# Kernel tuning notes

Hardware: AMD Instinct MI355X
Metric: run time of the kernel (lower is better)

## Reference

```python
import jax, jax.numpy as jnp
import numpy as np

EPS = 1e-8


def setup_inputs() -> dict:
    key = jax.random.key(0)
    ks = jax.random.split(key, 7)
    B, H, S, D = 4, 16, 4096, 64
    query = jax.random.normal(ks[0], (B, H, S, D), dtype=jnp.float32)
    k_in = jax.random.normal(ks[1], (B, H, S, D), dtype=jnp.float32)
    value = jax.random.normal(ks[2], (B, H, S, D), dtype=jnp.float32)
    output = jax.random.normal(ks[3], (B, H, S, D), dtype=jnp.float32)
    betas = jax.random.normal(ks[4], (H, 1, D), dtype=jnp.float32)
    init_states = jax.random.normal(ks[5], (H, D, D), dtype=jnp.float32)
    init_z = jax.random.uniform(ks[6], (H, D), dtype=jnp.float32)
    return {"query": query, "key": k_in, "value": value, "output": output,
            "betas": betas, "init_states": init_states, "init_z": init_z}


def reference(query, key, value, output, betas, init_states, init_z):
    # ---- compute updates (delta rule) ----
    sigma_k = jax.nn.elu(key) + 1.0                       # [B,H,S,D]
    # retrieved_value = (sigma_k @ states) / (sigma_k @ z + eps)
    num = jnp.einsum('bhsd,hde->bhse', sigma_k, init_states)   # [B,H,S,D]
    den = jnp.einsum('bhsd,hd->bhs', sigma_k, init_z)[..., None] + EPS
    value_update = value - num / den                      # delta rule
    # memory_states = init_states + sigma_k^T @ value_update -> [B,H,D,D]
    memory_states = init_states[None] + jnp.einsum('bhsd,bhse->bhde', sigma_k, value_update)
    memory_z = init_z[None] + sigma_k.sum(axis=-2)        # [B,H,D]
    # ---- retrieve memory ----
    sigma_q = jax.nn.elu(query) + 1.0                     # [B,H,S,D]
    retrieved = jnp.einsum('bhsd,bhde->bhse', sigma_q, memory_states)
    norm = jnp.einsum('bhsd,bhd->bhs', sigma_q, memory_z)[..., None] + EPS
    memory_output = retrieved / norm                      # [B,H,S,D]
    # ---- sigmoid-gated blend ----
    gate = jax.nn.sigmoid(betas)                          # [H,1,D] broadcasts over B,S
    return gate * memory_output + (1.0 - gate) * output
```

## Files before the change

kernel.cpp:

```cpp
#include <hip/hip_runtime.h>
#include <hip/hip_bf16.h>


#define B_  4
#define H_  16
#define S_  4096
#define D_  64
#define BH_ 64
#define EPS_ 1e-8f

typedef __attribute__((ext_vector_type(8))) short bf16x8;
typedef __attribute__((ext_vector_type(4))) float f32x4;
typedef __attribute__((ext_vector_type(4))) unsigned short u16x4;

__device__ __forceinline__ unsigned short f2bf(float x) {
    union { float f; unsigned u; } v; v.f = x;
    return (unsigned short)((v.u + 0x7FFFu + ((v.u >> 16) & 1u)) >> 16);
}
__device__ __forceinline__ float elup1(float x) {
    return x > 0.0f ? x + 1.0f : __expf(x);
}
__device__ __forceinline__ f32x4 fzero() { f32x4 z = {0.f, 0.f, 0.f, 0.f}; return z; }

__global__ __launch_bounds__(256, 4) void k1_states(
    const float* __restrict__ Kp, const float* __restrict__ Vp,
    const float* __restrict__ W0, const float* __restrict__ Z0,
    float* __restrict__ Mpart, float* __restrict__ Zpart, int NS)
{
    const int bh = blockIdx.x / NS;
    const int p  = blockIdx.x % NS;
    const int h  = bh & (H_ - 1);
    const int tid  = threadIdx.x;
    const int lane = tid & 63;
    const int wave = tid >> 6;
    const int c16  = lane & 15;
    const int g4   = lane >> 4;

    __shared__ float Glds[4][16][68];

    int   col[4];
    float z0l[4];
    #pragma unroll
    for (int q = 0; q < 4; ++q) {
        col[q] = (((wave + q) & 3) << 4) + c16;
        z0l[q] = Z0[h * 64 + col[q]];
    }

    bf16x8 ones;
    #pragma unroll
    for (int j = 0; j < 8; ++j) ones[j] = (short)0x3F80;

    const size_t base   = (size_t)bh * S_ * D_;
    const int    schunk = S_ / NS;
    const int    nch    = schunk >> 5;

    f32x4 mp1[4], gac[4], zac = fzero();
    #pragma unroll
    for (int i = 0; i < 4; ++i) { mp1[i] = fzero(); gac[i] = fzero(); }

    #pragma unroll 1
    for (int c = wave; c < nch; c += 4) {
        const float* kr = Kp + base + (size_t)(p * schunk + c * 32) * D_;
        const float* vr = Vp + base + (size_t)(p * schunk + c * 32) * D_;

        float kf[4][8];
        #pragma unroll
        for (int q = 0; q < 4; ++q)
        #pragma unroll
        for (int j = 0; j < 8; ++j)
            kf[q][j] = kr[(g4 * 8 + j) * 64 + col[q]];

        float den[8];
        #pragma unroll
        for (int j = 0; j < 8; ++j) den[j] = 0.f;
        #pragma unroll
        for (int q = 0; q < 4; ++q)
        #pragma unroll
        for (int j = 0; j < 8; ++j) {
            float s = elup1(kf[q][j]);
            kf[q][j] = s;
            den[j] += s * z0l[q];
        }
        #pragma unroll
        for (int j = 0; j < 8; ++j) {
            float d = den[j];
            d += __shfl_xor(d, 1); d += __shfl_xor(d, 2);
            d += __shfl_xor(d, 4); d += __shfl_xor(d, 8);
            den[j] = __builtin_amdgcn_rcpf(d + EPS_);
        }

        bf16x8 aown, skbS[4];
        #pragma unroll
        for (int j = 0; j < 8; ++j) aown[j] = (short)f2bf(kf[0][j]);
        #pragma unroll
        for (int q = 0; q < 4; ++q)
        #pragma unroll
        for (int j = 0; j < 8; ++j)
            skbS[q][j] = (short)f2bf(kf[q][j] * den[j]);

        float vf[4][8];
        #pragma unroll
        for (int nt = 0; nt < 4; ++nt)
        #pragma unroll
        for (int j = 0; j < 8; ++j)
            vf[nt][j] = vr[(g4 * 8 + j) * 64 + nt * 16 + c16];
        bf16x8 vbf[4];
        #pragma unroll
        for (int nt = 0; nt < 4; ++nt)
        #pragma unroll
        for (int j = 0; j < 8; ++j) vbf[nt][j] = (short)f2bf(vf[nt][j]);

        zac = __builtin_amdgcn_mfma_f32_16x16x32_bf16(aown, ones, zac, 0, 0, 0);
        #pragma unroll
        for (int nt = 0; nt < 4; ++nt)
            mp1[nt] = __builtin_amdgcn_mfma_f32_16x16x32_bf16(aown, vbf[nt], mp1[nt], 0, 0, 0);
        #pragma unroll
        for (int q = 0; q < 4; ++q)
            gac[q] = __builtin_amdgcn_mfma_f32_16x16x32_bf16(aown, skbS[q], gac[q], 0, 0, 0);
    }

    #pragma unroll
    for (int q = 0; q < 4; ++q)
    #pragma unroll
    for (int r = 0; r < 4; ++r)
        Glds[wave][g4 * 4 + r][(((wave + q) & 3) << 4) + c16] = gac[q][r];

    bf16x8 ag[2];
    #pragma unroll
    for (int kk = 0; kk < 2; ++kk)
    #pragma unroll
    for (int j = 0; j < 8; ++j)
        ag[kk][j] = (short)f2bf(Glds[wave][c16][kk * 32 + g4 * 8 + j]);

    f32x4 gw[4];
    #pragma unroll
    for (int nt = 0; nt < 4; ++nt) {
        f32x4 t = fzero();
        #pragma unroll
        for (int kk = 0; kk < 2; ++kk) {
            bf16x8 wb;
            #pragma unroll
            for (int j = 0; j < 8; ++j)
                wb[j] = (short)f2bf(W0[(size_t)h * 4096 + (kk * 32 + g4 * 8 + j) * 64 + nt * 16 + c16]);
            t = __builtin_amdgcn_mfma_f32_16x16x32_bf16(ag[kk], wb, t, 0, 0, 0);
        }
        gw[nt] = t;
    }

    #pragma unroll
    for (int nt = 0; nt < 4; ++nt)
    #pragma unroll
    for (int r = 0; r < 4; ++r)
        Glds[wave][g4 * 4 + r][nt * 16 + c16] = mp1[nt][r] - gw[nt][r];

    float* mout = Mpart + ((size_t)p * BH_ + bh) * 4096 + wave * 1024;
    #pragma unroll
    for (int q2 = 0; q2 < 4; ++q2) {
        f32x4 v = *(const f32x4*)&Glds[wave][q2 * 4 + g4][c16 * 4];
        *(f32x4*)(mout + q2 * 256 + lane * 4) = v;
    }

    if (c16 == 0) {
        #pragma unroll
        for (int r = 0; r < 4; ++r)
            Zpart[((size_t)p * BH_ + bh) * 64 + wave * 16 + g4 * 4 + r] = zac[r];
    }
}

__global__ void k_reduce(const float* __restrict__ Mpart, const float* __restrict__ Zpart,
                         const float* __restrict__ W0, const float* __restrict__ Z0,
                         unsigned short* __restrict__ MfinT, float* __restrict__ Zfin, int NS)
{
    const int bh = blockIdx.x >> 2, q = blockIdx.x & 3;
    const int h = bh & (H_ - 1), t = threadIdx.x;
    __shared__ float Ml[16][65];

    const int o = q * 1024 + t * 4;
    f32x4 s = *(const f32x4*)(W0 + (size_t)h * 4096 + o);
    for (int p = 0; p < NS; ++p)
        s = s + *(const f32x4*)(Mpart + ((size_t)p * BH_ + bh) * 4096 + o);
    const int dl = t >> 4, e0 = (t & 15) * 4;
    #pragma unroll
    for (int j = 0; j < 4; ++j) Ml[dl][e0 + j] = s[j];
    __syncthreads();

    const int e = t >> 2, dd0 = (t & 3) * 4;
    u16x4 w;
    #pragma unroll
    for (int j = 0; j < 4; ++j) w[j] = f2bf(Ml[dd0 + j][e]);
    *(u16x4*)(MfinT + (size_t)bh * 4096 + e * 64 + q * 16 + dd0) = w;

    if (q == 0 && t < 64) {
        float zs = Z0[h * 64 + t];
        for (int p = 0; p < NS; ++p) zs += Zpart[((size_t)p * BH_ + bh) * 64 + t];
        Zfin[bh * 64 + t] = zs;
    }
}

__global__ __launch_bounds__(256, 4) void k2_out(
    const float* __restrict__ Qp, const float* __restrict__ Op,
    const float* __restrict__ Bp, const unsigned short* __restrict__ MfinT,
    const float* __restrict__ Zfin, float* __restrict__ Out, int NS2)
{
    const int bh = blockIdx.x / NS2;
    const int p  = blockIdx.x % NS2;
    const int h  = bh & (H_ - 1);
    const int tid = threadIdx.x, lane = tid & 63, wave = tid >> 6;
    const int c16 = lane & 15, g4 = lane >> 4;

    float mzv[2][8];
    #pragma unroll
    for (int kk = 0; kk < 2; ++kk) {
        f32x4 a = *(const f32x4*)(Zfin + bh * 64 + kk * 32 + g4 * 8);
        f32x4 b = *(const f32x4*)(Zfin + bh * 64 + kk * 32 + g4 * 8 + 4);
        #pragma unroll
        for (int j = 0; j < 4; ++j) { mzv[kk][j] = a[j]; mzv[kk][4 + j] = b[j]; }
    }

    bf16x8 mf[4][2];
    #pragma unroll
    for (int et = 0; et < 4; ++et)
    #pragma unroll
    for (int kk = 0; kk < 2; ++kk)
        mf[et][kk] = *(const bf16x8*)(MfinT + (size_t)bh * 4096 + (et * 16 + c16) * 64 + kk * 32 + g4 * 8);

    float gate[4][4];
    #pragma unroll
    for (int et = 0; et < 4; ++et)
    #pragma unroll
    for (int r = 0; r < 4; ++r) {
        float b = Bp[h * 64 + et * 16 + g4 * 4 + r];
        gate[et][r] = 1.0f / (1.0f + __expf(-b));
    }

    const size_t base = (size_t)bh * S_ * D_;
    const int schunk = S_ / NS2, ngroups = schunk / 32;

    for (int g = wave; g < ngroups; g += 4) {
        const int row0 = p * schunk + g * 32;

        float sq[2][2][8];
        #pragma unroll
        for (int st = 0; st < 2; ++st) {
            const float* qr = Qp + base + (size_t)(row0 + st * 16 + c16) * D_;
            #pragma unroll
            for (int kk = 0; kk < 2; ++kk) {
                f32x4 a = *(const f32x4*)(qr + kk * 32 + g4 * 8);
                f32x4 b = *(const f32x4*)(qr + kk * 32 + g4 * 8 + 4);
                #pragma unroll
                for (int j = 0; j < 4; ++j) {
                    sq[st][kk][j]     = elup1(a[j]);
                    sq[st][kk][4 + j] = elup1(b[j]);
                }
            }
        }

        float n0 = 0.f, n1 = 0.f;
        #pragma unroll
        for (int kk = 0; kk < 2; ++kk)
        #pragma unroll
        for (int j = 0; j < 8; ++j) {
            n0 += sq[0][kk][j] * mzv[kk][j];
            n1 += sq[1][kk][j] * mzv[kk][j];
        }
        n0 += __shfl_xor(n0, 16); n0 += __shfl_xor(n0, 32);
        n1 += __shfl_xor(n1, 16); n1 += __shfl_xor(n1, 32);
        const float rn0 = __builtin_amdgcn_rcpf(n0 + EPS_);
        const float rn1 = __builtin_amdgcn_rcpf(n1 + EPS_);

        bf16x8 sqf[2][2];
        #pragma unroll
        for (int st = 0; st < 2; ++st)
        #pragma unroll
        for (int kk = 0; kk < 2; ++kk) {
            bf16x8 f;
            #pragma unroll
            for (int j = 0; j < 8; ++j) f[j] = (short)f2bf(sq[st][kk][j]);
            sqf[st][kk] = f;
        }

        f32x4 acc[2][4];
        #pragma unroll
        for (int st = 0; st < 2; ++st)
        #pragma unroll
        for (int et = 0; et < 4; ++et) {
            f32x4 t = __builtin_amdgcn_mfma_f32_16x16x32_bf16(mf[et][0], sqf[st][0], fzero(), 0, 0, 0);
            acc[st][et] = __builtin_amdgcn_mfma_f32_16x16x32_bf16(mf[et][1], sqf[st][1], t, 0, 0, 0);
        }

        #pragma unroll
        for (int st = 0; st < 2; ++st) {
            const float rn = st ? rn1 : rn0;
            const size_t roff = base + (size_t)(row0 + st * 16 + c16) * D_;
            #pragma unroll
            for (int et = 0; et < 4; ++et) {
                f32x4 o4 = *(const f32x4*)(Op + roff + et * 16 + g4 * 4);
                f32x4 w;
                #pragma unroll
                for (int r = 0; r < 4; ++r) {
                    float t = acc[st][et][r] * rn;
                    w[r] = o4[r] + gate[et][r] * (t - o4[r]);
                }
                *(f32x4*)(Out + roff + et * 16 + g4 * 4) = w;
            }
        }
    }
}

extern "C" void kernel_launch(void* const* d_in, const int* in_sizes, int n_in,
                              void* d_out, int out_size, void* d_ws, size_t ws_size,
                              hipStream_t stream)
{
    const float* Q  = (const float*)d_in[0];
    const float* K  = (const float*)d_in[1];
    const float* V  = (const float*)d_in[2];
    const float* O  = (const float*)d_in[3];
    const float* Bt = (const float*)d_in[4];
    const float* W0 = (const float*)d_in[5];
    const float* Z0 = (const float*)d_in[6];
    float* Out = (float*)d_out;

    int NS = 16;
    auto need = [](int ns) -> size_t {
        return sizeof(float) * ((size_t)ns * BH_ * 4096 + (size_t)ns * BH_ * 64 + BH_ * 64) +
               sizeof(unsigned short) * (size_t)BH_ * 4096;
    };
    while (NS > 1 && need(NS) > ws_size) NS >>= 1;

    float* Mpart = (float*)d_ws;
    float* Zpart = Mpart + (size_t)NS * BH_ * 4096;
    float* Zfin  = Zpart + (size_t)NS * BH_ * 64;
    unsigned short* MfinT = (unsigned short*)(Zfin + (size_t)BH_ * 64);

    hipLaunchKernelGGL(k1_states, dim3(BH_ * NS), dim3(256), 0, stream,
                       K, V, W0, Z0, Mpart, Zpart, NS);
    hipLaunchKernelGGL(k_reduce, dim3(BH_ * 4), dim3(256), 0, stream,
                       Mpart, Zpart, W0, Z0, MfinT, Zfin, NS);
    hipLaunchKernelGGL(k2_out, dim3(BH_ * 32), dim3(256), 0, stream,
                       Q, O, Bt, MfinT, Zfin, Out, 32);
}
```

Baseline: 89.18 us.

## Split kernels into single-wave blocks and hoist loads for memory-level parallelism

Both the state-accumulation kernel and the output kernel now launch 64-thread single-wave blocks, with four times as many blocks, instead of 256-thread blocks. The state kernel hoists the value loads ahead of the elu/denominator math and processes two chunks per loop iteration. The output kernel gives each wave one 32-row group and issues all query and output loads up front. The aim is more independent blocks and more loads in flight to hide memory latency, at the cost of more block-scheduling overhead and higher register pressure.

```diff
diff --git a/kernel.cpp b/kernel.cpp
--- a/kernel.cpp
+++ b/kernel.cpp
@@ -22,27 +22,28 @@
 }
 __device__ __forceinline__ f32x4 fzero() { f32x4 z = {0.f, 0.f, 0.f, 0.f}; return z; }
 
-__global__ __launch_bounds__(256, 4) void k1_states(
+__global__ __launch_bounds__(64, 4) void k1_states(
     const float* __restrict__ Kp, const float* __restrict__ Vp,
     const float* __restrict__ W0, const float* __restrict__ Z0,
     float* __restrict__ Mpart, float* __restrict__ Zpart, int NS)
 {
-    const int bh = blockIdx.x / NS;
-    const int p  = blockIdx.x % NS;
-    const int h  = bh & (H_ - 1);
-    const int tid  = threadIdx.x;
-    const int lane = tid & 63;
-    const int wave = tid >> 6;
+    const int bid = blockIdx.x;
+    const int w   = bid & 3;
+    const int t2  = bid >> 2;
+    const int bh  = t2 / NS;
+    const int p   = t2 % NS;
+    const int h   = bh & (H_ - 1);
+    const int lane = threadIdx.x;
     const int c16  = lane & 15;
     const int g4   = lane >> 4;
 
-    __shared__ float Glds[4][16][68];
+    __shared__ float Glds[16][68];
 
     int   col[4];
     float z0l[4];
     #pragma unroll
     for (int q = 0; q < 4; ++q) {
-        col[q] = (((wave + q) & 3) << 4) + c16;
+        col[q] = (((w + q) & 3) << 4) + c16;
         z0l[q] = Z0[h * 64 + col[q]];
     }
 
@@ -58,8 +59,7 @@
     #pragma unroll
     for (int i = 0; i < 4; ++i) { mp1[i] = fzero(); gac[i] = fzero(); }
 
-    #pragma unroll 1
-    for (int c = wave; c < nch; c += 4) {
+    auto do_chunk = [&](int c) {
         const float* kr = Kp + base + (size_t)(p * schunk + c * 32) * D_;
         const float* vr = Vp + base + (size_t)(p * schunk + c * 32) * D_;
 
@@ -69,6 +69,13 @@
         #pragma unroll
         for (int j = 0; j < 8; ++j)
             kf[q][j] = kr[(g4 * 8 + j) * 64 + col[q]];
+
+        float vf[4][8];
+        #pragma unroll
+        for (int nt = 0; nt < 4; ++nt)
+        #pragma unroll
+        for (int j = 0; j < 8; ++j)
+            vf[nt][j] = vr[(g4 * 8 + j) * 64 + nt * 16 + c16];
 
         float den[8];
         #pragma unroll
@@ -98,12 +105,6 @@
         for (int j = 0; j < 8; ++j)
             skbS[q][j] = (short)f2bf(kf[q][j] * den[j]);
 
-        float vf[4][8];
-        #pragma unroll
-        for (int nt = 0; nt < 4; ++nt)
-        #pragma unroll
-        for (int j = 0; j < 8; ++j)
-            vf[nt][j] = vr[(g4 * 8 + j) * 64 + nt * 16 + c16];
         bf16x8 vbf[4];
         #pragma unroll
         for (int nt = 0; nt < 4; ++nt)
@@ -117,20 +118,26 @@
         #pragma unroll
         for (int q = 0; q < 4; ++q)
             gac[q] = __builtin_amdgcn_mfma_f32_16x16x32_bf16(aown, skbS[q], gac[q], 0, 0, 0);
+    };
+
+    #pragma unroll 1
+    for (int c = w; c < nch; c += 8) {
+        do_chunk(c);
+        if (c + 4 < nch) do_chunk(c + 4);
     }
 
     #pragma unroll
     for (int q = 0; q < 4; ++q)
     #pragma unroll
     for (int r = 0; r < 4; ++r)
-        Glds[wave][g4 * 4 + r][(((wave + q) & 3) << 4) + c16] = gac[q][r];
+        Glds[g4 * 4 + r][(((w + q) & 3) << 4) + c16] = gac[q][r];
 
     bf16x8 ag[2];
     #pragma unroll
     for (int kk = 0; kk < 2; ++kk)
     #pragma unroll
     for (int j = 0; j < 8; ++j)
-        ag[kk][j] = (short)f2bf(Glds[wave][c16][kk * 32 + g4 * 8 + j]);
+        ag[kk][j] = (short)f2bf(Glds[c16][kk * 32 + g4 * 8 + j]);
 
     f32x4 gw[4];
     #pragma unroll
@@ -151,19 +158,19 @@
     for (int nt = 0; nt < 4; ++nt)
     #pragma unroll
     for (int r = 0; r < 4; ++r)
-        Glds[wave][g4 * 4 + r][nt * 16 + c16] = mp1[nt][r] - gw[nt][r];
-
-    float* mout = Mpart + ((size_t)p * BH_ + bh) * 4096 + wave * 1024;
+        Glds[g4 * 4 + r][nt * 16 + c16] = mp1[nt][r] - gw[nt][r];
+
+    float* mout = Mpart + ((size_t)p * BH_ + bh) * 4096 + w * 1024;
     #pragma unroll
     for (int q2 = 0; q2 < 4; ++q2) {
-        f32x4 v = *(const f32x4*)&Glds[wave][q2 * 4 + g4][c16 * 4];
+        f32x4 v = *(const f32x4*)&Glds[q2 * 4 + g4][c16 * 4];
         *(f32x4*)(mout + q2 * 256 + lane * 4) = v;
     }
 
     if (c16 == 0) {
         #pragma unroll
         for (int r = 0; r < 4; ++r)
-            Zpart[((size_t)p * BH_ + bh) * 64 + wave * 16 + g4 * 4 + r] = zac[r];
+            Zpart[((size_t)p * BH_ + bh) * 64 + w * 16 + g4 * 4 + r] = zac[r];
     }
 }
 
@@ -197,16 +204,44 @@
     }
 }
 
-__global__ __launch_bounds__(256, 4) void k2_out(
+__global__ __launch_bounds__(64, 4) void k2_out(
     const float* __restrict__ Qp, const float* __restrict__ Op,
     const float* __restrict__ Bp, const unsigned short* __restrict__ MfinT,
-    const float* __restrict__ Zfin, float* __restrict__ Out, int NS2)
+    const float* __restrict__ Zfin, float* __restrict__ Out)
 {
-    const int bh = blockIdx.x / NS2;
-    const int p  = blockIdx.x % NS2;
-    const int h  = bh & (H_ - 1);
-    const int tid = threadIdx.x, lane = tid & 63, wave = tid >> 6;
+    const int bid = blockIdx.x;
+    const int bh  = bid >> 7;
+    const int g   = bid & 127;
+    const int h   = bh & (H_ - 1);
+    const int lane = threadIdx.x;
     const int c16 = lane & 15, g4 = lane >> 4;
+    const int row0 = g * 32;
+    const size_t base = (size_t)bh * S_ * D_;
+
+    float sq[2][2][8];
+    #pragma unroll
+    for (int st = 0; st < 2; ++st) {
+        const float* qr = Qp + base + (size_t)(row0 + st * 16 + c16) * D_;
+        #pragma unroll
+        for (int kk = 0; kk < 2; ++kk) {
+            f32x4 a = *(const f32x4*)(qr + kk * 32 + g4 * 8);
+            f32x4 b = *(const f32x4*)(qr + kk * 32 + g4 * 8 + 4);
+            #pragma unroll
+            for (int j = 0; j < 4; ++j) {
+                sq[st][kk][j]     = a[j];
+                sq[st][kk][4 + j] = b[j];
+            }
+        }
+    }
+
+    f32x4 o4[2][4];
+    #pragma unroll
+    for (int st = 0; st < 2; ++st) {
+        const float* orow = Op + base + (size_t)(row0 + st * 16 + c16) * D_;
+        #pragma unroll
+        for (int et = 0; et < 4; ++et)
+            o4[st][et] = *(const f32x4*)(orow + et * 16 + g4 * 4);
+    }
 
     float mzv[2][8];
     #pragma unroll
@@ -216,14 +251,12 @@
         #pragma unroll
         for (int j = 0; j < 4; ++j) { mzv[kk][j] = a[j]; mzv[kk][4 + j] = b[j]; }
     }
-
     bf16x8 mf[4][2];
     #pragma unroll
     for (int et = 0; et < 4; ++et)
     #pragma unroll
     for (int kk = 0; kk < 2; ++kk)
         mf[et][kk] = *(const bf16x8*)(MfinT + (size_t)bh * 4096 + (et * 16 + c16) * 64 + kk * 32 + g4 * 8);
-
     float gate[4][4];
     #pragma unroll
     for (int et = 0; et < 4; ++et)
@@ -233,76 +266,55 @@
         gate[et][r] = 1.0f / (1.0f + __expf(-b));
     }
 
-    const size_t base = (size_t)bh * S_ * D_;
-    const int schunk = S_ / NS2, ngroups = schunk / 32;
-
-    for (int g = wave; g < ngroups; g += 4) {
-        const int row0 = p * schunk + g * 32;
-
-        float sq[2][2][8];
-        #pragma unroll
-        for (int st = 0; st < 2; ++st) {
-            const float* qr = Qp + base + (size_t)(row0 + st * 16 + c16) * D_;
+    float n0 = 0.f, n1 = 0.f;
+    #pragma unroll
+    for (int st = 0; st < 2; ++st)
+    #pragma unroll
+    for (int kk = 0; kk < 2; ++kk)
+    #pragma unroll
+    for (int j = 0; j < 8; ++j) {
+        float s = elup1(sq[st][kk][j]);
+        sq[st][kk][j] = s;
+        if (st == 0) n0 += s * mzv[kk][j]; else n1 += s * mzv[kk][j];
+    }
+    n0 += __shfl_xor(n0, 16); n0 += __shfl_xor(n0, 32);
+    n1 += __shfl_xor(n1, 16); n1 += __shfl_xor(n1, 32);
+    const float rn0 = __builtin_amdgcn_rcpf(n0 + EPS_);
+    const float rn1 = __builtin_amdgcn_rcpf(n1 + EPS_);
+
+    bf16x8 sqf[2][2];
+    #pragma unroll
+    for (int st = 0; st < 2; ++st)
+    #pragma unroll
+    for (int kk = 0; kk < 2; ++kk) {
+        bf16x8 f;
+        #pragma unroll
+        for (int j = 0; j < 8; ++j) f[j] = (short)f2bf(sq[st][kk][j]);
+        sqf[st][kk] = f;
+    }
+
+    f32x4 acc[2][4];
+    #pragma unroll
+    for (int st = 0; st < 2; ++st)
+    #pragma unroll
+    for (int et = 0; et < 4; ++et) {
+        f32x4 t = __builtin_amdgcn_mfma_f32_16x16x32_bf16(mf[et][0], sqf[st][0], fzero(), 0, 0, 0);
+        acc[st][et] = __builtin_amdgcn_mfma_f32_16x16x32_bf16(mf[et][1], sqf[st][1], t, 0, 0, 0);
+    }
+
+    #pragma unroll
+    for (int st = 0; st < 2; ++st) {
+        const float rn = st ? rn1 : rn0;
+        const size_t roff = base + (size_t)(row0 + st * 16 + c16) * D_;
+        #pragma unroll
+        for (int et = 0; et < 4; ++et) {
+            f32x4 wv;
             #pragma unroll
-            for (int kk = 0; kk < 2; ++kk) {
-                f32x4 a = *(const f32x4*)(qr + kk * 32 + g4 * 8);
-                f32x4 b = *(const f32x4*)(qr + kk * 32 + g4 * 8 + 4);
-                #pragma unroll
-                for (int j = 0; j < 4; ++j) {
-                    sq[st][kk][j]     = elup1(a[j]);
-                    sq[st][kk][4 + j] = elup1(b[j]);
-                }
+            for (int r = 0; r < 4; ++r) {
+                float t = acc[st][et][r] * rn;
+                wv[r] = o4[st][et][r] + gate[et][r] * (t - o4[st][et][r]);
             }
-        }
-
-        float n0 = 0.f, n1 = 0.f;
-        #pragma unroll
-        for (int kk = 0; kk < 2; ++kk)
-        #pragma unroll
-        for (int j = 0; j < 8; ++j) {
-            n0 += sq[0][kk][j] * mzv[kk][j];
-            n1 += sq[1][kk][j] * mzv[kk][j];
-        }
-        n0 += __shfl_xor(n0, 16); n0 += __shfl_xor(n0, 32);
-        n1 += __shfl_xor(n1, 16); n1 += __shfl_xor(n1, 32);
-        const float rn0 = __builtin_amdgcn_rcpf(n0 + EPS_);
-        const float rn1 = __builtin_amdgcn_rcpf(n1 + EPS_);
-
-        bf16x8 sqf[2][2];
-        #pragma unroll
-        for (int st = 0; st < 2; ++st)
-        #pragma unroll
-        for (int kk = 0; kk < 2; ++kk) {
-            bf16x8 f;
-            #pragma unroll
-            for (int j = 0; j < 8; ++j) f[j] = (short)f2bf(sq[st][kk][j]);
-            sqf[st][kk] = f;
-        }
-
-        f32x4 acc[2][4];
-        #pragma unroll
-        for (int st = 0; st < 2; ++st)
-        #pragma unroll
-        for (int et = 0; et < 4; ++et) {
-            f32x4 t = __builtin_amdgcn_mfma_f32_16x16x32_bf16(mf[et][0], sqf[st][0], fzero(), 0, 0, 0);
-            acc[st][et] = __builtin_amdgcn_mfma_f32_16x16x32_bf16(mf[et][1], sqf[st][1], t, 0, 0, 0);
-        }
-
-        #pragma unroll
-        for (int st = 0; st < 2; ++st) {
-            const float rn = st ? rn1 : rn0;
-            const size_t roff = base + (size_t)(row0 + st * 16 + c16) * D_;
-            #pragma unroll
-            for (int et = 0; et < 4; ++et) {
-                f32x4 o4 = *(const f32x4*)(Op + roff + et * 16 + g4 * 4);
-                f32x4 w;
-                #pragma unroll
-                for (int r = 0; r < 4; ++r) {
-                    float t = acc[st][et][r] * rn;
-                    w[r] = o4[r] + gate[et][r] * (t - o4[r]);
-                }
-                *(f32x4*)(Out + roff + et * 16 + g4 * 4) = w;
-            }
+            *(f32x4*)(Out + roff + et * 16 + g4 * 4) = wv;
         }
     }
 }
@@ -332,10 +344,10 @@
     float* Zfin  = Zpart + (size_t)NS * BH_ * 64;
     unsigned short* MfinT = (unsigned short*)(Zfin + (size_t)BH_ * 64);
 
-    hipLaunchKernelGGL(k1_states, dim3(BH_ * NS), dim3(256), 0, stream,
+    hipLaunchKernelGGL(k1_states, dim3(BH_ * NS * 4), dim3(64), 0, stream,
                        K, V, W0, Z0, Mpart, Zpart, NS);
     hipLaunchKernelGGL(k_reduce, dim3(BH_ * 4), dim3(256), 0, stream,
                        Mpart, Zpart, W0, Z0, MfinT, Zfin, NS);
-    hipLaunchKernelGGL(k2_out, dim3(BH_ * 32), dim3(256), 0, stream,
-                       Q, O, Bt, MfinT, Zfin, Out, 32);
-}
+    hipLaunchKernelGGL(k2_out, dim3(BH_ * 128), dim3(64), 0, stream,
+                       Q, O, Bt, MfinT, Zfin, Out);
+}
```

After: 91.42 us. 2.5% more time.
